# Performance work log

Hardware: AMD Instinct MI355X
Metric: run time of the kernel (lower is better)

Reference implementation:

```python
import jax, jax.numpy as jnp
import numpy as np

SIDE = 128
BATCH = 16


def setup_inputs() -> dict:
    key = jax.random.key(0)
    k1, k2 = jax.random.split(key)
    vol = jax.random.uniform(k1, (SIDE, SIDE, SIDE), dtype=jnp.float32)
    # random proper rotation matrices via QR of gaussian matrices
    a = jax.random.normal(k2, (BATCH, 3, 3), dtype=jnp.float32)
    q, r = jnp.linalg.qr(a)
    d = jnp.sign(jnp.diagonal(r, axis1=-2, axis2=-1))
    rotmat = q * d[:, None, :]
    return {"rotmat": rotmat, "vol": vol, "proj_axis": 3}


def _trilinear_sample(vol, grid):
    """torch.nn.functional.grid_sample (3D, bilinear/trilinear, align_corners=True,
    padding_mode='zeros') for a single-channel volume.

    vol:  [D, H, W] float
    grid: [B, N, 3] with (x, y, z) in [-1, 1]; x indexes W, y indexes H, z indexes D
    returns [B, N]
    """
    D, H, W = vol.shape
    vol_flat = vol.reshape(-1)

    def unnorm(c, size):
        return (c + 1.0) * 0.5 * (size - 1)

    ix = unnorm(grid[..., 0], W)
    iy = unnorm(grid[..., 1], H)
    iz = unnorm(grid[..., 2], D)

    x0 = jnp.floor(ix); x1 = x0 + 1.0
    y0 = jnp.floor(iy); y1 = y0 + 1.0
    z0 = jnp.floor(iz); z1 = z0 + 1.0

    wx = (x1 - ix, ix - x0)
    wy = (y1 - iy, iy - y0)
    wz = (z1 - iz, iz - z0)
    xs = (x0, x1); ys = (y0, y1); zs = (z0, z1)

    out = jnp.zeros(grid.shape[:-1], dtype=vol.dtype)
    for cz in range(2):
        for cy in range(2):
            for cx in range(2):
                xi = xs[cx].astype(jnp.int32)
                yi = ys[cy].astype(jnp.int32)
                zi = zs[cz].astype(jnp.int32)
                valid = ((xi >= 0) & (xi < W) & (yi >= 0) & (yi < H)
                         & (zi >= 0) & (zi < D))
                xc = jnp.clip(xi, 0, W - 1)
                yc = jnp.clip(yi, 0, H - 1)
                zc = jnp.clip(zi, 0, D - 1)
                idx = (zc * H + yc) * W + xc
                v = jnp.where(valid, vol_flat[idx], 0.0)
                out = out + v * (wx[cx] * wy[cy] * wz[cz])
    return out


def reference(rotmat, vol, proj_axis):
    S = vol.shape[0]
    B = rotmat.shape[0]
    lin = jnp.linspace(-1.0, 1.0, S, dtype=vol.dtype)
    # torch.meshgrid default is 'ij' indexing; coords stacked as [y, x, z]
    x, y, z = jnp.meshgrid(lin, lin, lin, indexing='ij')
    coords = jnp.stack([y, x, z], axis=-1).reshape(-1, 3)  # [S^3, 3]
    # pytorch3d Rotate.transform_points: points @ R  (batched)
    rot_coords = jnp.einsum('nc,bcd->bnd', coords, rotmat)  # [B, S^3, 3]
    samples = _trilinear_sample(vol, rot_coords)            # [B, S^3]
    rot_vol = samples.reshape(B, S, S, S)
    projection = jnp.sum(rot_vol, axis=proj_axis)           # [B, S, S]
    return projection[:, None, :, :]                        # [B, 1, S, S]
```

## Files before the change

kernel.cpp:

```cpp
#include <hip/hip_runtime.h>

#define S    128
#define SS   (S * S)
#define PW   136
#define PWH  (PW * PW)
#define PAD  4
#define VOXN (PW * PW * PW)
#define NT0  (VOXN / 256)
#define HT   68
#define HTS  69

__device__ __forceinline__ unsigned q8(const float v) {
    return (unsigned)(v * 255.0f + 0.5f);
}

__device__ __forceinline__ float fetch_padded(const float* __restrict__ vol,
                                              int x, int y, int z) {
    const int xm = x - PAD, ym = y - PAD, zm = z - PAD;
    if (((unsigned)xm < 128u) & ((unsigned)ym < 128u) & ((unsigned)zm < 128u))
        return vol[(zm * S + ym) * S + xm];
    return 0.0f;
}

__global__ __launch_bounds__(256) void oct0_build_kernel(
    const float* __restrict__ vol, uint2* __restrict__ pq,
    float* __restrict__ out)
{
    const int t = blockIdx.x * 256 + threadIdx.x;
    if (t < 16 * SS) out[t] = 0.0f;
    const int x = t % PW;
    const int r = t / PW;
    const int y = r % PW;
    const int z = r / PW;
    const unsigned w0 = q8(fetch_padded(vol, x,     y,     z))
                      | (q8(fetch_padded(vol, x + 1, y,     z)) << 8)
                      | (q8(fetch_padded(vol, x,     y + 1, z)) << 16)
                      | (q8(fetch_padded(vol, x + 1, y + 1, z)) << 24);
    const unsigned w1 = q8(fetch_padded(vol, x,     y,     z + 1))
                      | (q8(fetch_padded(vol, x + 1, y,     z + 1)) << 8)
                      | (q8(fetch_padded(vol, x,     y + 1, z + 1)) << 16)
                      | (q8(fetch_padded(vol, x + 1, y + 1, z + 1)) << 24);
    pq[t] = make_uint2(w0, w1);
}

__device__ __forceinline__ unsigned perm_swap12(unsigned w) {
    return (w & 0xFF0000FFu) | ((w & 0x0000FF00u) << 8) | ((w & 0x00FF0000u) >> 8);
}

__global__ __launch_bounds__(256) void oct_transpose_kernel(
    const uint2* __restrict__ pq0, uint2* __restrict__ pq)
{
    const int bid = blockIdx.x;
    const int cp  = 1 + bid / (PW * 4);
    const int rem = bid % (PW * 4);
    const int s   = rem / 4;
    const int tl  = rem % 4;
    const int fo  = (tl >> 1) * HT;
    const int mo  = (tl & 1) * HT;

    __shared__ unsigned Tx[HT * HTS];
    __shared__ unsigned Ty[HT * HTS];

    for (int idx = threadIdx.x; idx < HT * HT; idx += 256) {
        const int xx = idx % HT;
        const int ff = idx / HT;
        const int F  = fo + ff;
        const int X  = mo + xx;
        const int src = (cp == 1) ? (s * PW + F) * PW + X
                                  : (F * PW + s) * PW + X;
        const uint2 q = pq0[src];
        Tx[ff * HTS + xx] = q.x;
        Ty[ff * HTS + xx] = q.y;
    }
    __syncthreads();

    uint2* dst = pq + (size_t)cp * VOXN + s * PWH;
    for (int idx = threadIdx.x; idx < HT * HT; idx += 256) {
        const int ff = idx % HT;
        const int XX = idx / HT;
        const unsigned w0 = Tx[ff * HTS + XX];
        const unsigned w1 = Ty[ff * HTS + XX];
        unsigned o0, o1;
        if (cp == 1) {
            o0 = perm_swap12(w0);
            o1 = perm_swap12(w1);
        } else {
            o0 = (w0 & 0xFFu) | ((w1 & 0xFFu) << 8)
               | ((w0 & 0xFF00u) << 8) | ((w1 & 0xFF00u) << 16);
            o1 = ((w0 >> 16) & 0xFFu) | (((w1 >> 16) & 0xFFu) << 8)
               | (((w0 >> 24) & 0xFFu) << 16) | (w1 & 0xFF000000u);
        }
        dst[(mo + XX) * PW + (fo + ff)] = make_uint2(o0, o1);
    }
}

struct Ray {
    float ix0, iy0, iz0, ux, uy, uz;
    int kmin, kmax;
};

__device__ __forceinline__ Ray make_ray(const float* __restrict__ rot,
                                        int b, int i, int j, int seg) {
    const float* Rb = rot + b * 9;
    const float r00 = Rb[0], r01 = Rb[1], r02 = Rb[2];
    const float r10 = Rb[3], r11 = Rb[4], r12 = Rb[5];
    const float r20 = Rb[6], r21 = Rb[7], r22 = Rb[8];

    const float step = 2.0f / 127.0f;
    const float li = -1.0f + step * (float)i;
    const float lj = -1.0f + step * (float)j;

    Ray ry;
    ry.ix0 = (lj * r00 + li * r10 - r20 + 1.0f) * 63.5f + (float)PAD;
    ry.iy0 = (lj * r01 + li * r11 - r21 + 1.0f) * 63.5f + (float)PAD;
    ry.iz0 = (lj * r02 + li * r12 - r22 + 1.0f) * 63.5f + (float)PAD;
    ry.ux = r20; ry.uy = r21; ry.uz = r22;

    float klo = 0.0f, khi = 127.0f;
    const float lo = (float)(PAD - 1), hi = (float)(PAD + 128);
    if (fabsf(ry.ux) > 1e-7f) {
        float a = (lo - ry.ix0) / ry.ux, c = (hi - ry.ix0) / ry.ux;
        klo = fmaxf(klo, fminf(a, c)); khi = fminf(khi, fmaxf(a, c));
    } else if (ry.ix0 <= lo || ry.ix0 >= hi) { klo = 1e9f; khi = -1e9f; }
    if (fabsf(ry.uy) > 1e-7f) {
        float a = (lo - ry.iy0) / ry.uy, c = (hi - ry.iy0) / ry.uy;
        klo = fmaxf(klo, fminf(a, c)); khi = fminf(khi, fmaxf(a, c));
    } else if (ry.iy0 <= lo || ry.iy0 >= hi) { klo = 1e9f; khi = -1e9f; }
    if (fabsf(ry.uz) > 1e-7f) {
        float a = (lo - ry.iz0) / ry.uz, c = (hi - ry.iz0) / ry.uz;
        klo = fmaxf(klo, fminf(a, c)); khi = fminf(khi, fmaxf(a, c));
    } else if (ry.iz0 <= lo || ry.iz0 >= hi) { klo = 1e9f; khi = -1e9f; }

    ry.kmin = seg * 32; ry.kmax = seg * 32 + 31;
    if (klo <= khi) {
        ry.kmin = max(ry.kmin, (int)floorf(klo) - 1);
        ry.kmax = min(ry.kmax, (int)ceilf(khi) + 1);
    } else {
        ry.kmax = ry.kmin - 1;
    }
    return ry;
}

__device__ __forceinline__ void permute_ray(const Ray& ry, int sel,
    float& px0, float& py0, float& pz0, float& pux, float& puy, float& puz)
{
    px0 = ry.ix0; py0 = ry.iy0; pz0 = ry.iz0;
    pux = ry.ux;  puy = ry.uy;  puz = ry.uz;
    if (sel == 1) {
        px0 = ry.iy0; py0 = ry.ix0;
        pux = ry.uy;  puy = ry.ux;
    } else if (sel == 2) {
        px0 = ry.iz0; py0 = ry.ix0; pz0 = ry.iy0;
        pux = ry.uz;  puy = ry.ux;  puz = ry.uy;
    }
}

__global__ __launch_bounds__(256) void projector_oct(
    const float* __restrict__ rot,
    const uint2* __restrict__ pq,
    float* __restrict__ out)
{
    const int blk  = blockIdx.x;
    const int b    = blk >> 8;
    const int seg  = (blk >> 6) & 3;
    const int tile = blk & 63;
    const int tY   = tile >> 3, tX = tile & 7;

    const int wave = threadIdx.x >> 6;
    const int lane = threadIdx.x & 63;
    const int i = tY * 16 + (wave >> 1) * 8 + (lane >> 3);
    const int j = tX * 16 + (wave & 1) * 8 + (lane & 7);

    const Ray ry = make_ray(rot, b, i, j, seg);

    const float ax = fabsf(ry.ux), ay = fabsf(ry.uy), az = fabsf(ry.uz);
    const int sel = (ax <= ay && ax <= az) ? 0 : ((ay <= az) ? 1 : 2);
    float pf0, pm0, pa0, uf, um, ua;
    permute_ray(ry, sel, pf0, pm0, pa0, uf, um, ua);
    const uint2* __restrict__ vq = pq + (size_t)sel * VOXN;

    float acc = 0.0f;
    #pragma unroll 4
    for (int k = ry.kmin; k <= ry.kmax; ++k) {
        const float kk = (float)k;
        const float pf = fmaf(kk, uf, pf0);
        const float pm = fmaf(kk, um, pm0);
        const float pa = fmaf(kk, ua, pa0);

        const float ff_ = floorf(pf), mf_ = floorf(pm), af_ = floorf(pa);
        const float ff = pf - ff_, fm = pm - mf_, fa = pa - af_;
        const int f0 = (int)ff_, m0 = (int)mf_, a0 = (int)af_;

        const uint2 q = vq[(a0 * PW + m0) * PW + f0];
        const unsigned q0 = q.x, q1 = q.y;

        const float v00a = (float)(q0 & 0xffu);
        const float v10a = (float)((q0 >> 8) & 0xffu);
        const float v01a = (float)((q0 >> 16) & 0xffu);
        const float v11a = (float)(q0 >> 24);
        const float v00b = (float)(q1 & 0xffu);
        const float v10b = (float)((q1 >> 8) & 0xffu);
        const float v01b = (float)((q1 >> 16) & 0xffu);
        const float v11b = (float)(q1 >> 24);

        const float e0a = fmaf(ff, v10a - v00a, v00a);
        const float e1a = fmaf(ff, v11a - v01a, v01a);
        const float wa  = fmaf(fm, e1a - e0a, e0a);
        const float e0b = fmaf(ff, v10b - v00b, v00b);
        const float e1b = fmaf(ff, v11b - v01b, v01b);
        const float wb  = fmaf(fm, e1b - e0b, e0b);
        acc += fmaf(fa, wb - wa, wa);
    }

    atomicAdd(&out[(b << 14) + (i << 7) + j], acc * (1.0f / 255.0f));
}

#define TW   68
#define NTT  (PW * 9)

__global__ __launch_bounds__(256) void quad_build_kernel(
    const float* __restrict__ vol, unsigned* __restrict__ pq)
{
    const int bid = blockIdx.x;
    if (bid < NT0) {
        const int t = bid * 256 + threadIdx.x;
        const int x = t % PW;
        const int r = t / PW;
        const int y = r % PW;
        const int z = r / PW;
        const unsigned v0 = q8(fetch_padded(vol, x,     y,     z));
        const unsigned v1 = q8(fetch_padded(vol, x + 1, y,     z));
        const unsigned v2 = q8(fetch_padded(vol, x,     y + 1, z));
        const unsigned v3 = q8(fetch_padded(vol, x + 1, y + 1, z));
        pq[t] = v0 | (v1 << 8) | (v2 << 16) | (v3 << 24);
        return;
    }
    const int bid2 = bid - NT0;
    const int cp   = 1 + bid2 / NTT;
    const int rem  = bid2 % NTT;
    const int s    = rem / 9;
    const int tile = rem % 9;
    const int c0   = (tile / 3) * 64;
    const int x0   = (tile % 3) * 64;

    __shared__ unsigned char LT[68 * TW];
    for (int idx = threadIdx.x; idx < 65 * 65; idx += 256) {
        const int rr = idx / 65;
        const int cc = idx - rr * 65;
        const int fr = c0 + rr;
        const int xr = x0 + cc;
        const float v = (cp == 1) ? fetch_padded(vol, xr, fr, s)
                                  : fetch_padded(vol, xr, s, fr);
        LT[cc * TW + rr] = (unsigned char)q8(v);
    }
    __syncthreads();

    const int yc = threadIdx.x & 63;
    const int xb = threadIdx.x >> 6;
    const int yg = c0 + yc;
    if (yg >= PW) return;
    unsigned* dst = pq + (size_t)cp * VOXN + s * PWH + yg;
    #pragma unroll 4
    for (int m = 0; m < 16; ++m) {
        const int ox = xb * 16 + m;
        const int xg = x0 + ox;
        if (xg >= PW) break;
        const unsigned v00 = LT[ox * TW + yc];
        const unsigned v01 = LT[ox * TW + yc + 1];
        const unsigned v10 = LT[(ox + 1) * TW + yc];
        const unsigned v11 = LT[(ox + 1) * TW + yc + 1];
        dst[xg * PW] = v00 | (v01 << 8) | (v10 << 16) | (v11 << 24);
    }
}

__global__ __launch_bounds__(256) void projector_quad(
    const float* __restrict__ rot, const unsigned* __restrict__ pq,
    float* __restrict__ out)
{
    const int blk  = blockIdx.x;
    const int b    = blk >> 8;
    const int seg  = (blk >> 6) & 3;
    const int tile = blk & 63;
    const int tY   = tile >> 3, tX = tile & 7;
    const int wave = threadIdx.x >> 6;
    const int lane = threadIdx.x & 63;
    const int i = tY * 16 + (wave >> 1) * 8 + (lane >> 3);
    const int j = tX * 16 + (wave & 1) * 8 + (lane & 7);

    const Ray ry = make_ray(rot, b, i, j, seg);
    const float ax = fabsf(ry.ux), ay = fabsf(ry.uy), az = fabsf(ry.uz);
    const int sel = (ax <= ay && ax <= az) ? 0 : ((ay <= az) ? 1 : 2);
    float pf0, pm0, pa0, uf, um, ua;
    permute_ray(ry, sel, pf0, pm0, pa0, uf, um, ua);
    const unsigned* __restrict__ vq = pq + sel * VOXN;

    float acc = 0.0f;
    #pragma unroll 4
    for (int k = ry.kmin; k <= ry.kmax; ++k) {
        const float kk = (float)k;
        const float pf = fmaf(kk, uf, pf0);
        const float pm = fmaf(kk, um, pm0);
        const float pa = fmaf(kk, ua, pa0);
        const float ff_ = floorf(pf), mf_ = floorf(pm), af_ = floorf(pa);
        const float ff = pf - ff_, fm = pm - mf_, fa = pa - af_;
        const int idx = ((int)af_ * PW + (int)mf_) * PW + (int)ff_;
        const unsigned q0 = vq[idx];
        const unsigned q1 = vq[idx + PWH];
        const float v00a = (float)(q0 & 0xffu);
        const float v10a = (float)((q0 >> 8) & 0xffu);
        const float v01a = (float)((q0 >> 16) & 0xffu);
        const float v11a = (float)(q0 >> 24);
        const float v00b = (float)(q1 & 0xffu);
        const float v10b = (float)((q1 >> 8) & 0xffu);
        const float v01b = (float)((q1 >> 16) & 0xffu);
        const float v11b = (float)(q1 >> 24);
        const float e0a = fmaf(ff, v10a - v00a, v00a);
        const float e1a = fmaf(ff, v11a - v01a, v01a);
        const float wa  = fmaf(fm, e1a - e0a, e0a);
        const float e0b = fmaf(ff, v10b - v00b, v00b);
        const float e1b = fmaf(ff, v11b - v01b, v01b);
        const float wb  = fmaf(fm, e1b - e0b, e0b);
        acc += fmaf(fa, wb - wa, wa);
    }
    atomicAdd(&out[(b << 14) + (i << 7) + j], acc * (1.0f / 255.0f));
}

__global__ __launch_bounds__(256) void projector_f32(
    const float* __restrict__ rot, const float* __restrict__ vol,
    float* __restrict__ out)
{
    const int pix = blockIdx.x * 256 + threadIdx.x;
    const int b = pix >> 14, rem = pix & 16383;
    const int i = rem >> 7, j = rem & 127;
    const float* Rb = rot + b * 9;
    const float step = 2.0f / 127.0f;
    const float li = -1.0f + step * (float)i;
    const float lj = -1.0f + step * (float)j;
    const float ix0 = (lj * Rb[0] + li * Rb[3] - Rb[6] + 1.0f) * 63.5f;
    const float iy0 = (lj * Rb[1] + li * Rb[4] - Rb[7] + 1.0f) * 63.5f;
    const float iz0 = (lj * Rb[2] + li * Rb[5] - Rb[8] + 1.0f) * 63.5f;
    const float ux = Rb[6], uy = Rb[7], uz = Rb[8];
    float acc = 0.0f;
    for (int k = 0; k < 128; ++k) {
        const float kk = (float)k;
        const float ix = fmaf(kk, ux, ix0), iy = fmaf(kk, uy, iy0), iz = fmaf(kk, uz, iz0);
        const float xf = floorf(ix), yf = floorf(iy), zf = floorf(iz);
        const float fx = ix - xf, fy = iy - yf, fz = iz - zf;
        const int x0 = (int)xf, y0 = (int)yf, z0 = (int)zf;
        const int x1 = x0 + 1, y1 = y0 + 1, z1 = z0 + 1;
        const bool vx0 = (unsigned)x0 < 128u, vx1 = (unsigned)x1 < 128u;
        const bool vy0 = (unsigned)y0 < 128u, vy1 = (unsigned)y1 < 128u;
        const bool vz0 = (unsigned)z0 < 128u, vz1 = (unsigned)z1 < 128u;
        const float v000 = (vx0 && vy0 && vz0) ? vol[(z0 * S + y0) * S + x0] : 0.0f;
        const float v001 = (vx1 && vy0 && vz0) ? vol[(z0 * S + y0) * S + x1] : 0.0f;
        const float v010 = (vx0 && vy1 && vz0) ? vol[(z0 * S + y1) * S + x0] : 0.0f;
        const float v011 = (vx1 && vy1 && vz0) ? vol[(z0 * S + y1) * S + x1] : 0.0f;
        const float v100 = (vx0 && vy0 && vz1) ? vol[(z1 * S + y0) * S + x0] : 0.0f;
        const float v101 = (vx1 && vy0 && vz1) ? vol[(z1 * S + y0) * S + x1] : 0.0f;
        const float v110 = (vx0 && vy1 && vz1) ? vol[(z1 * S + y1) * S + x0] : 0.0f;
        const float v111 = (vx1 && vy1 && vz1) ? vol[(z1 * S + y1) * S + x1] : 0.0f;
        const float c00 = v000 + fx * (v001 - v000);
        const float c01 = v010 + fx * (v011 - v010);
        const float c10 = v100 + fx * (v101 - v100);
        const float c11 = v110 + fx * (v111 - v110);
        const float c0 = c00 + fy * (c01 - c00);
        const float c1 = c10 + fy * (c11 - c10);
        acc += c0 + fz * (c1 - c0);
    }
    out[pix] = acc;
}

extern "C" void kernel_launch(void* const* d_in, const int* in_sizes, int n_in,
                              void* d_out, int out_size, void* d_ws, size_t ws_size,
                              hipStream_t stream) {
    const float* rot = (const float*)d_in[0];
    const float* vol = (const float*)d_in[1];
    float* out = (float*)d_out;

    const size_t need_oct  = (size_t)3 * VOXN * 8;
    const size_t need_quad = (size_t)3 * VOXN * 4;

    if (ws_size >= need_oct) {
        uint2* pq = (uint2*)d_ws;
        oct0_build_kernel<<<NT0, 256, 0, stream>>>(vol, pq, out);
        oct_transpose_kernel<<<2 * PW * 4, 256, 0, stream>>>(pq, pq);
        projector_oct<<<4096, 256, 0, stream>>>(rot, pq, out);
    } else if (ws_size >= need_quad) {
        unsigned* pq = (unsigned*)d_ws;
        hipMemsetAsync(out, 0, (size_t)out_size * sizeof(float), stream);
        quad_build_kernel<<<NT0 + 2 * NTT, 256, 0, stream>>>(vol, pq);
        projector_quad<<<4096, 256, 0, stream>>>(rot, pq, out);
    } else {
        projector_f32<<<(16 * SS) / 256, 256, 0, stream>>>(rot, vol, out);
    }
}
```

Baseline: 102.7 us.

## Fuse octet build and transposed-copy kernels into one launch from raw volume

The separate build and transpose kernels become one kernel. The two transposed octet layouts are now built straight from the float volume through a shared-memory tile, so they no longer read the first packed layout. This drops a kernel launch and the serial dependency between the two build stages, letting all three layouts be produced in parallel. The inner projector loop unroll also goes from 4 to 8, which may raise register pressure.

```diff
diff --git a/kernel.cpp b/kernel.cpp
--- a/kernel.cpp
+++ b/kernel.cpp
@@ -8,7 +8,7 @@
 #define VOXN (PW * PW * PW)
 #define NT0  (VOXN / 256)
 #define HT   68
-#define HTS  69
+#define RS   69
 
 __device__ __forceinline__ unsigned q8(const float v) {
     return (unsigned)(v * 255.0f + 0.5f);
@@ -22,75 +22,65 @@
     return 0.0f;
 }
 
-__global__ __launch_bounds__(256) void oct0_build_kernel(
+__global__ __launch_bounds__(256) void oct_build_all_kernel(
     const float* __restrict__ vol, uint2* __restrict__ pq,
     float* __restrict__ out)
 {
-    const int t = blockIdx.x * 256 + threadIdx.x;
-    if (t < 16 * SS) out[t] = 0.0f;
-    const int x = t % PW;
-    const int r = t / PW;
-    const int y = r % PW;
-    const int z = r / PW;
-    const unsigned w0 = q8(fetch_padded(vol, x,     y,     z))
-                      | (q8(fetch_padded(vol, x + 1, y,     z)) << 8)
-                      | (q8(fetch_padded(vol, x,     y + 1, z)) << 16)
-                      | (q8(fetch_padded(vol, x + 1, y + 1, z)) << 24);
-    const unsigned w1 = q8(fetch_padded(vol, x,     y,     z + 1))
-                      | (q8(fetch_padded(vol, x + 1, y,     z + 1)) << 8)
-                      | (q8(fetch_padded(vol, x,     y + 1, z + 1)) << 16)
-                      | (q8(fetch_padded(vol, x + 1, y + 1, z + 1)) << 24);
-    pq[t] = make_uint2(w0, w1);
-}
-
-__device__ __forceinline__ unsigned perm_swap12(unsigned w) {
-    return (w & 0xFF0000FFu) | ((w & 0x0000FF00u) << 8) | ((w & 0x00FF0000u) >> 8);
-}
-
-__global__ __launch_bounds__(256) void oct_transpose_kernel(
-    const uint2* __restrict__ pq0, uint2* __restrict__ pq)
-{
+    __shared__ float LT[2][RS * RS];
+
     const int bid = blockIdx.x;
-    const int cp  = 1 + bid / (PW * 4);
-    const int rem = bid % (PW * 4);
-    const int s   = rem / 4;
-    const int tl  = rem % 4;
-    const int fo  = (tl >> 1) * HT;
-    const int mo  = (tl & 1) * HT;
-
-    __shared__ unsigned Tx[HT * HTS];
-    __shared__ unsigned Ty[HT * HTS];
-
-    for (int idx = threadIdx.x; idx < HT * HT; idx += 256) {
-        const int xx = idx % HT;
-        const int ff = idx / HT;
+
+    if (bid < NT0) {
+        const int t = bid * 256 + threadIdx.x;
+        if (t < 16 * SS) out[t] = 0.0f;
+        const int x = t % PW;
+        const int r = t / PW;
+        const int y = r % PW;
+        const int z = r / PW;
+        const unsigned w0 = q8(fetch_padded(vol, x,     y,     z))
+                          | (q8(fetch_padded(vol, x + 1, y,     z)) << 8)
+                          | (q8(fetch_padded(vol, x,     y + 1, z)) << 16)
+                          | (q8(fetch_padded(vol, x + 1, y + 1, z)) << 24);
+        const unsigned w1 = q8(fetch_padded(vol, x,     y,     z + 1))
+                          | (q8(fetch_padded(vol, x + 1, y,     z + 1)) << 8)
+                          | (q8(fetch_padded(vol, x,     y + 1, z + 1)) << 16)
+                          | (q8(fetch_padded(vol, x + 1, y + 1, z + 1)) << 24);
+        pq[t] = make_uint2(w0, w1);
+        return;
+    }
+
+    const int bid2 = bid - NT0;
+    const int cp   = 1 + bid2 / (PW * 4);
+    const int rem  = bid2 % (PW * 4);
+    const int s    = rem / 4;
+    const int tl   = rem % 4;
+    const int fo   = (tl >> 1) * HT;
+    const int mo   = (tl & 1) * HT;
+
+    for (int idx = threadIdx.x; idx < 2 * RS * RS; idx += 256) {
+        const int sl = idx / (RS * RS);
+        const int r2 = idx - sl * (RS * RS);
+        const int mm = r2 % RS;
+        const int ff = r2 / RS;
         const int F  = fo + ff;
-        const int X  = mo + xx;
-        const int src = (cp == 1) ? (s * PW + F) * PW + X
-                                  : (F * PW + s) * PW + X;
-        const uint2 q = pq0[src];
-        Tx[ff * HTS + xx] = q.x;
-        Ty[ff * HTS + xx] = q.y;
+        const int X  = mo + mm;
+        const float v = (cp == 1) ? fetch_padded(vol, X, F, s + sl)
+                                  : fetch_padded(vol, X, s + sl, F);
+        LT[sl][mm * RS + ff] = v;
     }
     __syncthreads();
 
     uint2* dst = pq + (size_t)cp * VOXN + s * PWH;
     for (int idx = threadIdx.x; idx < HT * HT; idx += 256) {
         const int ff = idx % HT;
-        const int XX = idx / HT;
-        const unsigned w0 = Tx[ff * HTS + XX];
-        const unsigned w1 = Ty[ff * HTS + XX];
-        unsigned o0, o1;
-        if (cp == 1) {
-            o0 = perm_swap12(w0);
-            o1 = perm_swap12(w1);
-        } else {
-            o0 = (w0 & 0xFFu) | ((w1 & 0xFFu) << 8)
-               | ((w0 & 0xFF00u) << 8) | ((w1 & 0xFF00u) << 16);
-            o1 = ((w0 >> 16) & 0xFFu) | (((w1 >> 16) & 0xFFu) << 8)
-               | (((w0 >> 24) & 0xFFu) << 16) | (w1 & 0xFF000000u);
-        }
-        dst[(mo + XX) * PW + (fo + ff)] = make_uint2(o0, o1);
+        const int mm = idx / HT;
+        const float* t0 = &LT[0][mm * RS + ff];
+        const float* t1 = &LT[1][mm * RS + ff];
+        const unsigned w0 = q8(t0[0]) | (q8(t0[1]) << 8)
+                          | (q8(t0[RS]) << 16) | (q8(t0[RS + 1]) << 24);
+        const unsigned w1 = q8(t1[0]) | (q8(t1[1]) << 8)
+                          | (q8(t1[RS]) << 16) | (q8(t1[RS + 1]) << 24);
+        dst[(mo + mm) * PW + (fo + ff)] = make_uint2(w0, w1);
     }
 }
 
@@ -180,7 +170,7 @@
     const uint2* __restrict__ vq = pq + (size_t)sel * VOXN;
 
     float acc = 0.0f;
-    #pragma unroll 4
+    #pragma unroll 8
     for (int k = ry.kmin; k <= ry.kmax; ++k) {
         const float kk = (float)k;
         const float pf = fmaf(kk, uf, pf0);
@@ -382,8 +372,7 @@
 
     if (ws_size >= need_oct) {
         uint2* pq = (uint2*)d_ws;
-        oct0_build_kernel<<<NT0, 256, 0, stream>>>(vol, pq, out);
-        oct_transpose_kernel<<<2 * PW * 4, 256, 0, stream>>>(pq, pq);
+        oct_build_all_kernel<<<NT0 + 2 * PW * 4, 256, 0, stream>>>(vol, pq, out);
         projector_oct<<<4096, 256, 0, stream>>>(rot, pq, out);
     } else if (ws_size >= need_quad) {
         unsigned* pq = (unsigned*)d_ws;
```

Result: slower. 134.2 us (+30.6%).
